# Optimization experiments

Measured on AMD Instinct MI355X. Metric: run time of the kernel, lower is better.

## Reference

```python
import jax, jax.numpy as jnp
import numpy as np

H = 64    # encoder/decoder hidden size
L = 10    # num_lags
D = 128   # input_dim (features)
OUT = 5   # out_dim
B = 8192


def lstm_cell(x, h, c, Wih, Whh, bih, bhh):
    # torch nn.LSTM gate order: i, f, g, o
    g = x @ Wih.T + bih + h @ Whh.T + bhh
    i, f, gg, o = jnp.split(g, 4, axis=-1)
    c = jax.nn.sigmoid(f) * c + jax.nn.sigmoid(i) * jnp.tanh(gg)
    h = jax.nn.sigmoid(o) * jnp.tanh(c)
    return h, c


def setup_inputs() -> dict:
    key = jax.random.key(0)
    ks = jax.random.split(key, 24)
    rn = lambda k, s, sc=0.05: jax.random.normal(k, s, jnp.float32) * sc
    return {
        "x": rn(ks[0], (B, L, D), 1.0),
        "y_hist": rn(ks[1], (B, L, OUT), 1.0),
        "h0_enc": rn(ks[2], (B, H), 0.1),
        "c0_enc": rn(ks[3], (B, H), 0.1),
        "h0_dec": rn(ks[4], (B, H), 0.1),
        "c0_dec": rn(ks[5], (B, H), 0.1),
        # encoder attention: Linear(2H+L -> 1)
        "enc_attn_w": rn(ks[6], (1, 2 * H + L)),
        "enc_attn_b": rn(ks[7], (1,)),
        # encoder LSTM
        "enc_Wih": rn(ks[8], (4 * H, D)),
        "enc_Whh": rn(ks[9], (4 * H, H)),
        "enc_bih": rn(ks[10], (4 * H,)),
        "enc_bhh": rn(ks[11], (4 * H,)),
        # decoder attention MLP: Linear(3H -> H), tanh, Linear(H -> 1)
        "dec_attn_w1": rn(ks[12], (H, 3 * H)),
        "dec_attn_b1": rn(ks[13], (H,)),
        "dec_attn_w2": rn(ks[14], (1, H)),
        "dec_attn_b2": rn(ks[15], (1,)),
        # decoder LSTM (input = out_dim)
        "dec_Wih": rn(ks[16], (4 * H, OUT)),
        "dec_Whh": rn(ks[17], (4 * H, H)),
        "dec_bih": rn(ks[18], (4 * H,)),
        "dec_bhh": rn(ks[19], (4 * H,)),
        # fc: Linear(H+OUT -> OUT)  (weight .normal_() in torch -> std 1)
        "fc_w": rn(ks[20], (OUT, H + OUT), 1.0),
        "fc_b": rn(ks[21], (OUT,)),
        # fc_out: Linear(2H -> OUT)
        "fcout_w": rn(ks[22], (OUT, 2 * H)),
        "fcout_b": rn(ks[23], (OUT,)),
    }


def reference(x, y_hist, h0_enc, c0_enc, h0_dec, c0_dec,
              enc_attn_w, enc_attn_b, enc_Wih, enc_Whh, enc_bih, enc_bhh,
              dec_attn_w1, dec_attn_b1, dec_attn_w2, dec_attn_b2,
              dec_Wih, dec_Whh, dec_bih, dec_bhh, fc_w, fc_b, fcout_w, fcout_b):
    # ---- encoder (input attention over features) ----
    # Linear([h; c; x_feat_series]) = wh.h + wc.c + wx.x_series + b
    wh, wc, wx = enc_attn_w[0, :H], enc_attn_w[0, H:2 * H], enc_attn_w[0, 2 * H:]
    score_x = jnp.einsum('bdl,l->bd', jnp.transpose(x, (0, 2, 1)), wx)  # [B, D]

    def enc_step(carry, x_t):
        h, c = carry
        scores = (h @ wh + c @ wc)[:, None] + score_x + enc_attn_b[0]   # [B, D]
        at = jax.nn.softmax(scores, axis=1)
        wi = at * x_t                                                   # [B, D]
        h, c = lstm_cell(wi, h, c, enc_Wih, enc_Whh, enc_bih, enc_bhh)
        return (h, c), h

    _, enc_seq = jax.lax.scan(enc_step, (h0_enc, c0_enc), jnp.transpose(x, (1, 0, 2)))
    x_enc = jnp.transpose(enc_seq, (1, 0, 2))                           # [B, L, H]

    # ---- decoder (temporal attention over encoded lags) ----
    W1h, W1c, W1x = dec_attn_w1[:, :H], dec_attn_w1[:, H:2 * H], dec_attn_w1[:, 2 * H:]
    pre = jnp.einsum('ble,he->blh', x_enc, W1x)                         # [B, L, H]
    w2 = dec_attn_w2[0]

    def dec_step(carry, y_t):
        h, c, _ = carry
        z = jnp.tanh(pre + (h @ W1h.T + c @ W1c.T + dec_attn_b1)[:, None, :])
        scores = z @ w2 + dec_attn_b2[0]                                # [B, L]
        at = jax.nn.softmax(scores, axis=1)
        ctx = jnp.einsum('bl,ble->be', at, x_enc)                       # [B, H]
        y_tilde = jnp.concatenate([ctx, y_t], axis=1) @ fc_w.T + fc_b   # [B, OUT]
        h, c = lstm_cell(y_tilde, h, c, dec_Wih, dec_Whh, dec_bih, dec_bhh)
        return (h, c, ctx), None

    (h, c, ctx), _ = jax.lax.scan(
        dec_step, (h0_dec, c0_dec, jnp.zeros_like(h0_dec)),
        jnp.transpose(y_hist, (1, 0, 2)))
    out = jnp.concatenate([h, ctx], axis=1) @ fcout_w.T + fcout_b       # [B, OUT]
    return out
```

## Files before the change

### kernel.cpp

```cpp
#include <hip/hip_runtime.h>

#define B_  8192
#define L_  10
#define D_  128
#define H_  64
#define OUT_ 5

typedef _Float16 h2 __attribute__((ext_vector_type(2)));
typedef _Float16 f16x8 __attribute__((ext_vector_type(8)));
typedef float f32x4 __attribute__((ext_vector_type(4)));
typedef unsigned int uint;

#define WS_ENCPK   0
#define WS_ENCB    24576
#define WS_DECY2   24832
#define WS_DECPK   26112
#define WS_DECB    34304
#define WS_W1HCP   34560
#define WS_W1XP    38656

__device__ __forceinline__ float sigmf(float x){ return 1.f/(1.f+__expf(-x)); }
__device__ __forceinline__ float tanhf_(float x){ return 1.f - 2.f/(1.f+__expf(2.f*x)); }
__device__ __forceinline__ uint pack_rtz(float a, float b){
  return __builtin_bit_cast(uint, __builtin_amdgcn_cvt_pkrtz(a, b));
}
__device__ __forceinline__ uint pack_rtn(float a, float b){
  h2 v; v.x = (_Float16)a; v.y = (_Float16)b;
  return __builtin_bit_cast(uint, v);
}
__device__ __forceinline__ float2 unpk(uint u){
  h2 v = __builtin_bit_cast(h2, u);
  return make_float2((float)v.x, (float)v.y);
}

union U4 { uint u[4]; uint4 q; f16x8 v; };

__global__ void prep_kernel(const float* __restrict__ encWih, const float* __restrict__ encWhh,
                            const float* __restrict__ encbih, const float* __restrict__ encbhh,
                            const float* __restrict__ decWih, const float* __restrict__ decWhh,
                            const float* __restrict__ decbih, const float* __restrict__ decbhh,
                            const float* __restrict__ w1, float* __restrict__ wsf)
{
  uint* ws = (uint*)wsf;
  int stride = gridDim.x * blockDim.x;
  int tid0 = blockIdx.x * blockDim.x + threadIdx.x;

  for (int idx = tid0; idx < 96*64; idx += stride) {
    int kp = idx >> 6, l = idx & 63;
    uint4 o; uint* op = (uint*)&o;
    #pragma unroll
    for (int q=0;q<4;++q){
      int j = q*64 + l;
      int k0 = 2*kp, k1 = 2*kp+1;
      float a = (k0 < 128) ? encWih[j*128 + k0] : encWhh[j*64 + (k0-128)];
      float b = (k1 < 128) ? encWih[j*128 + k1] : encWhh[j*64 + (k1-128)];
      op[q] = pack_rtn(a,b);
    }
    ((uint4*)(ws + WS_ENCPK))[idx] = o;
  }
  for (int idx = tid0; idx < 256; idx += stride) {
    int l = idx >> 2, q = idx & 3, j = q*64+l;
    wsf[WS_ENCB+idx] = encbih[j] + encbhh[j];
  }
  for (int idx = tid0; idx < 4*64; idx += stride) {
    int i = idx >> 6, l = idx & 63;
    uint4 o; uint* op = (uint*)&o;
    #pragma unroll
    for (int q=0;q<4;++q){
      int j = q*64 + l;
      int k0 = 2*i, k1 = 2*i+1;
      float a = (k0 < 5) ? decWih[j*5 + k0] : 0.f;
      float b = (k1 < 5) ? decWih[j*5 + k1] : 0.f;
      op[q] = pack_rtn(a,b);
    }
    ((uint4*)(ws + WS_DECY2))[idx] = o;
  }
  for (int idx = tid0; idx < 32*64; idx += stride) {
    int ep = idx >> 6, l = idx & 63;
    uint4 o; uint* op = (uint*)&o;
    #pragma unroll
    for (int q=0;q<4;++q){
      int j = q*64 + l;
      op[q] = pack_rtn(decWhh[j*64 + 2*ep], decWhh[j*64 + 2*ep+1]);
    }
    ((uint4*)(ws + WS_DECPK))[idx] = o;
  }
  for (int idx = tid0; idx < 256; idx += stride) {
    int l = idx >> 2, q = idx & 3, j = q*64+l;
    wsf[WS_DECB+idx] = decbih[j] + decbhh[j];
  }
  for (int idx = tid0; idx < 32*64; idx += stride) {
    int ep = idx >> 6, l = idx & 63;
    uint2 o;
    o.x = pack_rtn(w1[l*192 + 2*ep],      w1[l*192 + 2*ep+1]);
    o.y = pack_rtn(w1[l*192 + 64 + 2*ep], w1[l*192 + 64 + 2*ep+1]);
    ((uint2*)(ws + WS_W1HCP))[idx] = o;
  }
  for (int idx = tid0; idx < 32*64; idx += stride) {
    int ep = idx >> 6, l = idx & 63;
    ws[WS_W1XP + idx] = pack_rtn(w1[l*192 + 128 + 2*ep], w1[l*192 + 128 + 2*ep+1]);
  }
}

#define SM_HXE   0
#define SM_XES   4608
#define SM_TMPF  0
#define SM_TMPG  12800
#define SM_HXD   27648
#define SM_CXD   32256
#define SM_SRED  36864
#define SM_FXE   39424
#define SM_GXE   42624
#define SM_YBS   45824
#define SM_TOTAL 49024

__global__ __launch_bounds__(256, 2) void darnn_fused(
    const float* __restrict__ x, const float* __restrict__ enc_attn_w,
    const float* __restrict__ y_hist,
    const float* __restrict__ h0e, const float* __restrict__ c0e,
    const float* __restrict__ h0d, const float* __restrict__ c0d,
    const float* __restrict__ dec_attn_b1, const float* __restrict__ dec_attn_w2,
    const float* __restrict__ fc_w, const float* __restrict__ fc_b,
    const float* __restrict__ fcout_w, const float* __restrict__ fcout_b,
    const float* __restrict__ ws,
    float* __restrict__ out)
{
  const int tid = threadIdx.x;
  const int l   = tid & 63;
  const int w   = tid >> 6;
  const int col = l & 15;
  const int g   = l >> 4;
  const int b0  = blockIdx.x * 16;
  const int lw  = 16*w + col;
  const int u0  = 16*w + 4*g;

  const uint* wsu = (const uint*)ws;

  __shared__ __align__(16) char smem_[SM_TOTAL];
  _Float16 (*wiS)[16][136] = reinterpret_cast<_Float16(*)[16][136]>(smem_);
  uint     (*hxE)[16][36] = reinterpret_cast<uint(*)[16][36]>(smem_ + SM_HXE);
  _Float16 (*xeS)[16][72] = reinterpret_cast<_Float16(*)[16][72]>(smem_ + SM_XES);
  float* tmpF = (float*)(smem_ + SM_TMPF);
  float* tmpG = (float*)(smem_ + SM_TMPG);
  uint     (*hxD)[16][36] = reinterpret_cast<uint(*)[16][36]>(smem_ + SM_HXD);
  uint     (*cxD)[16][36] = reinterpret_cast<uint(*)[16][36]>(smem_ + SM_CXD);
  float* sred = (float*)(smem_ + SM_SRED);
  float* fxeS = (float*)(smem_ + SM_FXE);
  float* gxeS = (float*)(smem_ + SM_GXE);
  float* ybS  = (float*)(smem_ + SM_YBS);

  if (tid < 200){
    float4 yreg = *(const float4*)(y_hist + (size_t)b0*50 + tid*4);
    *(float4*)(ybS + tid*4) = yreg;
  }
  float4 hd4 = *(const float4*)(h0d + (size_t)(b0+col)*64 + u0);
  float4 cd4 = *(const float4*)(c0d + (size_t)(b0+col)*64 + u0);
  float4 he4 = *(const float4*)(h0e + (size_t)(b0+col)*64 + u0);
  float4 ce4 = *(const float4*)(c0e + (size_t)(b0+col)*64 + u0);

  f16x8 afr[4][4];
  #pragma unroll
  for (int im=0; im<4; ++im){
    #pragma unroll
    for (int kf=0; kf<4; ++kf){
      U4 cv;
      #pragma unroll
      for (int i=0;i<4;++i){
        int kp = kf*16 + g*4 + i;
        cv.u[i] = wsu[WS_ENCPK + (kp*64 + lw)*4 + im];
      }
      afr[im][kf] = cv.v;
    }
  }
  float bias[4][4];
  #pragma unroll
  for (int im=0; im<4; ++im)
    #pragma unroll
    for (int r=0; r<4; ++r)
      bias[im][r] = ws[WS_ENCB + (u0 + r)*4 + im];

  const int bb = tid >> 4;
  const int kc = tid & 15;
  const float* xb = x + (size_t)(b0+bb)*(L_*D_) + kc*8;

  float wxv[L_];
  #pragma unroll
  for (int t=0;t<L_;++t) wxv[t] = enc_attn_w[2*H_ + t];

  float s[8];
  #pragma unroll
  for (int j=0;j<8;++j) s[j]=0.f;
  #pragma unroll
  for (int t=0;t<L_;++t){
    float wx = wxv[t];
    float4 x0 = *(const float4*)(xb + t*D_);
    float4 x1 = *(const float4*)(xb + t*D_ + 4);
    s[0]+=x0.x*wx; s[1]+=x0.y*wx; s[2]+=x0.z*wx; s[3]+=x0.w*wx;
    s[4]+=x1.x*wx; s[5]+=x1.y*wx; s[6]+=x1.z*wx; s[7]+=x1.w*wx;
  }
  float m = s[0];
  #pragma unroll
  for (int j=1;j<8;++j) m = fmaxf(m, s[j]);
  m = fmaxf(m, __shfl_xor(m,1));
  m = fmaxf(m, __shfl_xor(m,2));
  m = fmaxf(m, __shfl_xor(m,4));
  m = fmaxf(m, __shfl_xor(m,8));
  float atw[8];
  float ss = 0.f;
  #pragma unroll
  for (int j=0;j<8;++j){ atw[j] = __expf(s[j]-m); ss += atw[j]; }
  ss += __shfl_xor(ss,1);
  ss += __shfl_xor(ss,2);
  ss += __shfl_xor(ss,4);
  ss += __shfl_xor(ss,8);
  float ainv = 1.f/ss;
  #pragma unroll
  for (int j=0;j<8;++j) atw[j] *= ainv;

  #pragma unroll
  for (int t=0;t<L_;++t){
    float4 x0 = *(const float4*)(xb + t*D_);
    float4 x1 = *(const float4*)(xb + t*D_ + 4);
    uint4 o;
    o.x = pack_rtz(atw[0]*x0.x, atw[1]*x0.y);
    o.y = pack_rtz(atw[2]*x0.z, atw[3]*x0.w);
    o.z = pack_rtz(atw[4]*x1.x, atw[5]*x1.y);
    o.w = pack_rtz(atw[6]*x1.z, atw[7]*x1.w);
    *(uint4*)&wiS[t][bb][kc*8] = o;
  }
  __syncthreads();

  uint2 gq[L_][4];
  #pragma unroll
  for (int t=0;t<L_;++t){
    U4 bu[4];
    #pragma unroll
    for (int kf=0;kf<4;++kf)
      bu[kf].q = *(const uint4*)&wiS[t][col][kf*32 + g*8];
    #pragma unroll
    for (int im=0;im<4;++im){
      f32x4 acc = { bias[im][0], bias[im][1], bias[im][2], bias[im][3] };
      #pragma unroll
      for (int kf=0;kf<4;++kf)
        acc = __builtin_amdgcn_mfma_f32_16x16x32_f16(afr[im][kf], bu[kf].v, acc, 0, 0, 0);
      gq[t][im] = make_uint2(pack_rtn(acc[0],acc[1]), pack_rtn(acc[2],acc[3]));
    }
  }
  __syncthreads();

  f16x8 aE[4][2];
  #pragma unroll
  for (int q=0;q<4;++q)
    #pragma unroll
    for (int kf=0;kf<2;++kf){
      U4 cv;
      #pragma unroll
      for (int i=0;i<4;++i)
        cv.u[i] = wsu[WS_ENCPK + ((64 + kf*16 + g*4 + i)*64 + lw)*4 + q];
      aE[q][kf] = cv.v;
    }

  float h[4], c[4], xer[L_][4];
  h[0]=he4.x; h[1]=he4.y; h[2]=he4.z; h[3]=he4.w;
  c[0]=ce4.x; c[1]=ce4.y; c[2]=ce4.z; c[3]=ce4.w;
  *(uint2*)&hxE[0][col][u0>>1] = make_uint2(pack_rtz(h[0],h[1]), pack_rtz(h[2],h[3]));
  __syncthreads();

  int p = 0;
  #pragma unroll
  for (int t=0; t<L_; ++t){
    f32x4 acc[4];
    #pragma unroll
    for (int q=0;q<4;++q){
      float2 u0f = unpk(gq[t][q].x), u1f = unpk(gq[t][q].y);
      acc[q][0]=u0f.x; acc[q][1]=u0f.y; acc[q][2]=u1f.x; acc[q][3]=u1f.y;
    }
    f16x8 hB[2];
    { U4 t0; t0.q = *(const uint4*)&hxE[p][col][g*4];      hB[0]=t0.v; }
    { U4 t1; t1.q = *(const uint4*)&hxE[p][col][16 + g*4]; hB[1]=t1.v; }

    #pragma unroll
    for (int q=0;q<4;++q){
      acc[q] = __builtin_amdgcn_mfma_f32_16x16x32_f16(aE[q][0], hB[0], acc[q], 0,0,0);
      acc[q] = __builtin_amdgcn_mfma_f32_16x16x32_f16(aE[q][1], hB[1], acc[q], 0,0,0);
    }
    #pragma unroll
    for (int r=0;r<4;++r){
      float ig=sigmf(acc[0][r]), fg=sigmf(acc[1][r]), gg=tanhf_(acc[2][r]), og=sigmf(acc[3][r]);
      c[r]=fg*c[r]+ig*gg;
      h[r]=og*tanhf_(c[r]);
      xer[t][r]=h[r];
    }
    uint2 hpk = make_uint2(pack_rtz(h[0],h[1]), pack_rtz(h[2],h[3]));
    *(uint2*)&xeS[t][col][u0] = hpk;
    *(uint2*)&hxE[p^1][col][u0>>1] = hpk;
    __syncthreads();
    p ^= 1;
  }

  f16x8 aX[2];
  #pragma unroll
  for (int kf=0;kf<2;++kf){
    U4 cv;
    #pragma unroll
    for (int i=0;i<4;++i) cv.u[i] = wsu[WS_W1XP + (kf*16 + g*4 + i)*64 + lw];
    aX[kf] = cv.v;
  }
  f32x4 preC[L_];
  #pragma unroll
  for (int lt=0;lt<L_;++lt){
    f32x4 a = {0.f,0.f,0.f,0.f};
    U4 bu0, bu1;
    bu0.q = *(const uint4*)&xeS[lt][col][g*8];
    bu1.q = *(const uint4*)&xeS[lt][col][32 + g*8];
    a = __builtin_amdgcn_mfma_f32_16x16x32_f16(aX[0], bu0.v, a, 0,0,0);
    a = __builtin_amdgcn_mfma_f32_16x16x32_f16(aX[1], bu1.v, a, 0,0,0);
    preC[lt] = a;
  }
  __syncthreads();

  {
    float fw1v[OUT_][4], gw1v[OUT_][4];
    #pragma unroll
    for (int o2=0;o2<OUT_;++o2)
      #pragma unroll
      for (int r=0;r<4;++r){
        fw1v[o2][r] = fc_w[o2*69 + u0 + r];
        gw1v[o2][r] = fcout_w[o2*128 + 64 + u0 + r];
      }
    #pragma unroll
    for (int lt=0;lt<L_;++lt){
      #pragma unroll
      for (int o2=0;o2<OUT_;++o2){
        float pf = fw1v[o2][0]*xer[lt][0] + fw1v[o2][1]*xer[lt][1]
                 + fw1v[o2][2]*xer[lt][2] + fw1v[o2][3]*xer[lt][3];
        float pg = gw1v[o2][0]*xer[lt][0] + gw1v[o2][1]*xer[lt][1]
                 + gw1v[o2][2]*xer[lt][2] + gw1v[o2][3]*xer[lt][3];
        pf += __shfl_xor(pf,16); pf += __shfl_xor(pf,32);
        pg += __shfl_xor(pg,16); pg += __shfl_xor(pg,32);
        if (g==0){
          tmpF[((lt*16+col)*OUT_+o2)*4 + w] = pf;
          tmpG[((lt*16+col)*OUT_+o2)*4 + w] = pg;
        }
      }
    }
  }
  __syncthreads();
  for (int idx=tid; idx<800; idx+=256){
    float4 f4 = *(const float4*)(tmpF + idx*4);
    float4 g4 = *(const float4*)(tmpG + idx*4);
    int o2 = idx % 5, rest = idx / 5;
    int b  = rest % 16, lt = rest / 16;
    fxeS[b*50 + lt*5 + o2] = f4.x+f4.y+f4.z+f4.w;
    gxeS[b*50 + lt*5 + o2] = g4.x+g4.y+g4.z+g4.w;
  }

  f16x8 aW1[4];
  #pragma unroll
  for (int kf=0;kf<4;++kf){
    U4 cv;
    #pragma unroll
    for (int i=0;i<4;++i){
      int ep = (kf&1)*16 + g*4 + i;
      cv.u[i] = wsu[WS_W1HCP + (ep*64 + lw)*2 + (kf>>1)];
    }
    aW1[kf] = cv.v;
  }
  f16x8 aGh[4][2];
  #pragma unroll
  for (int q=0;q<4;++q)
    #pragma unroll
    for (int kf=0;kf<2;++kf){
      U4 cv;
      #pragma unroll
      for (int i=0;i<4;++i)
        cv.u[i] = wsu[WS_DECPK + ((kf*16 + g*4 + i)*64 + lw)*4 + q];
      aGh[q][kf] = cv.v;
    }
  f16x8 aG0[4];
  #pragma unroll
  for (int q=0;q<4;++q){
    U4 cv;
    #pragma unroll
    for (int i=0;i<4;++i)
      cv.u[i] = (g==0) ? wsu[WS_DECY2 + (i*64 + lw)*4 + q] : 0u;
    aG0[q] = cv.v;
  }
  float4 bD[4];
  #pragma unroll
  for (int r=0;r<4;++r) bD[r] = *(const float4*)(ws + WS_DECB + (u0+r)*4);
  float4 b1v = *(const float4*)(dec_attn_b1 + u0);
  float4 w2v = *(const float4*)(dec_attn_w2 + u0);
  float fcbv[OUT_], fw2v[OUT_][OUT_];
  #pragma unroll
  for (int o2=0;o2<OUT_;++o2){
    fcbv[o2] = fc_b[o2];
    #pragma unroll
    for (int j=0;j<OUT_;++j) fw2v[o2][j] = fc_w[o2*69 + 64 + j];
  }

  h[0]=hd4.x; h[1]=hd4.y; h[2]=hd4.z; h[3]=hd4.w;
  c[0]=cd4.x; c[1]=cd4.y; c[2]=cd4.z; c[3]=cd4.w;
  *(uint2*)&hxD[0][col][u0>>1] = make_uint2(pack_rtz(h[0],h[1]), pack_rtz(h[2],h[3]));
  *(uint2*)&cxD[0][col][u0>>1] = make_uint2(pack_rtz(c[0],c[1]), pack_rtz(c[2],c[3]));
  __syncthreads();

  float at[L_];
  float inv = 0.f;
  p = 0;
  for (int t=0; t<L_; ++t){
    f16x8 hB[2], cB[2];
    { U4 t0; t0.q = *(const uint4*)&hxD[p][col][g*4];      hB[0]=t0.v; }
    { U4 t1; t1.q = *(const uint4*)&hxD[p][col][16 + g*4]; hB[1]=t1.v; }
    { U4 t2; t2.q = *(const uint4*)&cxD[p][col][g*4];      cB[0]=t2.v; }
    { U4 t3; t3.q = *(const uint4*)&cxD[p][col][16 + g*4]; cB[1]=t3.v; }

    f32x4 vb = { b1v.x, b1v.y, b1v.z, b1v.w };
    vb = __builtin_amdgcn_mfma_f32_16x16x32_f16(aW1[0], hB[0], vb, 0,0,0);
    vb = __builtin_amdgcn_mfma_f32_16x16x32_f16(aW1[1], hB[1], vb, 0,0,0);
    vb = __builtin_amdgcn_mfma_f32_16x16x32_f16(aW1[2], cB[0], vb, 0,0,0);
    vb = __builtin_amdgcn_mfma_f32_16x16x32_f16(aW1[3], cB[1], vb, 0,0,0);

    #pragma unroll
    for (int lt=0;lt<L_;++lt){
      float zp = tanhf_(preC[lt][0] + vb[0]) * w2v.x
               + tanhf_(preC[lt][1] + vb[1]) * w2v.y
               + tanhf_(preC[lt][2] + vb[2]) * w2v.z
               + tanhf_(preC[lt][3] + vb[3]) * w2v.w;
      zp += __shfl_xor(zp,16);
      zp += __shfl_xor(zp,32);
      at[lt] = zp;
    }
    if (g==0){
      #pragma unroll
      for (int lt=0;lt<L_;++lt) sred[(lt*16+col)*4 + w] = at[lt];
    }
    __syncthreads();
    #pragma unroll
    for (int lt=0;lt<L_;++lt){
      float4 s4 = *(const float4*)(sred + (lt*16+col)*4);
      at[lt] = s4.x + s4.y + s4.z + s4.w;
    }
    float mx = at[0];
    #pragma unroll
    for (int lt=1;lt<L_;++lt) mx = fmaxf(mx, at[lt]);
    float ssum = 0.f;
    #pragma unroll
    for (int lt=0;lt<L_;++lt){ at[lt] = __expf(at[lt]-mx); ssum += at[lt]; }
    inv = 1.f/ssum;

    U4 ycv; ycv.u[0]=0u; ycv.u[1]=0u; ycv.u[2]=0u; ycv.u[3]=0u;
    if (g==0){
      const float* fx = fxeS + col*50;
      const float* yb = ybS + col*50 + t*5;
      float yt[OUT_];
      #pragma unroll
      for (int o2=0;o2<OUT_;++o2){
        float sv = 0.f;
        #pragma unroll
        for (int lt=0;lt<L_;++lt) sv += at[lt]*fx[lt*5+o2];
        float v = sv*inv + fcbv[o2];
        #pragma unroll
        for (int j=0;j<OUT_;++j) v += yb[j]*fw2v[o2][j];
        yt[o2] = v;
      }
      ycv.u[0] = pack_rtn(yt[0], yt[1]);
      ycv.u[1] = pack_rtn(yt[2], yt[3]);
      ycv.u[2] = pack_rtn(yt[4], 0.f);
    }
    f32x4 accQ[4];
    #pragma unroll
    for (int q=0;q<4;++q){
      accQ[q][0]=((const float*)&bD[0])[q];
      accQ[q][1]=((const float*)&bD[1])[q];
      accQ[q][2]=((const float*)&bD[2])[q];
      accQ[q][3]=((const float*)&bD[3])[q];
    }
    #pragma unroll
    for (int q=0;q<4;++q){
      accQ[q] = __builtin_amdgcn_mfma_f32_16x16x32_f16(aG0[q], ycv.v, accQ[q], 0,0,0);
      accQ[q] = __builtin_amdgcn_mfma_f32_16x16x32_f16(aGh[q][0], hB[0], accQ[q], 0,0,0);
      accQ[q] = __builtin_amdgcn_mfma_f32_16x16x32_f16(aGh[q][1], hB[1], accQ[q], 0,0,0);
    }
    #pragma unroll
    for (int r=0;r<4;++r){
      float ig=sigmf(accQ[0][r]), fg=sigmf(accQ[1][r]), gg=tanhf_(accQ[2][r]), og=sigmf(accQ[3][r]);
      c[r]=fg*c[r]+ig*gg;
      h[r]=og*tanhf_(c[r]);
    }
    *(uint2*)&hxD[p^1][col][u0>>1] = make_uint2(pack_rtz(h[0],h[1]), pack_rtz(h[2],h[3]));
    *(uint2*)&cxD[p^1][col][u0>>1] = make_uint2(pack_rtz(c[0],c[1]), pack_rtz(c[2],c[3]));
    __syncthreads();
    p ^= 1;
  }

  {
    float fcA[OUT_][4];
    #pragma unroll
    for (int o2=0;o2<OUT_;++o2)
      #pragma unroll
      for (int r=0;r<4;++r) fcA[o2][r] = fcout_w[o2*128 + u0 + r];
    #pragma unroll
    for (int o2=0;o2<OUT_;++o2){
      float pv = fcA[o2][0]*h[0] + fcA[o2][1]*h[1] + fcA[o2][2]*h[2] + fcA[o2][3]*h[3];
      pv += __shfl_xor(pv,16);
      pv += __shfl_xor(pv,32);
      if (g==0) sred[(o2*16+col)*4 + w] = pv;
    }
  }
  __syncthreads();
  if (w==0 && g==0){
    const float* gx = gxeS + col*50;
    #pragma unroll
    for (int o2=0;o2<OUT_;++o2){
      float4 s4 = *(const float4*)(sred + (o2*16+col)*4);
      float sv = 0.f;
      #pragma unroll
      for (int lt=0;lt<L_;++lt) sv += at[lt]*gx[lt*5+o2];
      out[(size_t)(b0+col)*OUT_ + o2] = s4.x+s4.y+s4.z+s4.w + sv*inv + fcout_b[o2];
    }
  }
}

extern "C" void kernel_launch(void* const* d_in, const int* in_sizes, int n_in,
                              void* d_out, int out_size, void* d_ws, size_t ws_size,
                              hipStream_t stream) {
  const float* x          = (const float*)d_in[0];
  const float* y_hist     = (const float*)d_in[1];
  const float* h0_enc     = (const float*)d_in[2];
  const float* c0_enc     = (const float*)d_in[3];
  const float* h0_dec     = (const float*)d_in[4];
  const float* c0_dec     = (const float*)d_in[5];
  const float* enc_attn_w = (const float*)d_in[6];
  const float* enc_Wih    = (const float*)d_in[8];
  const float* enc_Whh    = (const float*)d_in[9];
  const float* enc_bih    = (const float*)d_in[10];
  const float* enc_bhh    = (const float*)d_in[11];
  const float* dec_attn_w1= (const float*)d_in[12];
  const float* dec_attn_b1= (const float*)d_in[13];
  const float* dec_attn_w2= (const float*)d_in[14];
  const float* dec_Wih    = (const float*)d_in[16];
  const float* dec_Whh    = (const float*)d_in[17];
  const float* dec_bih    = (const float*)d_in[18];
  const float* dec_bhh    = (const float*)d_in[19];
  const float* fc_w       = (const float*)d_in[20];
  const float* fc_b       = (const float*)d_in[21];
  const float* fcout_w    = (const float*)d_in[22];
  const float* fcout_b    = (const float*)d_in[23];
  float* ws = (float*)d_ws;
  float* out = (float*)d_out;

  hipLaunchKernelGGL(prep_kernel, dim3(128), dim3(256), 0, stream,
                     enc_Wih, enc_Whh, enc_bih, enc_bhh,
                     dec_Wih, dec_Whh, dec_bih, dec_bhh,
                     dec_attn_w1, ws);
  hipLaunchKernelGGL(darnn_fused, dim3(B_/16), dim3(256), 0, stream,
                     x, enc_attn_w, y_hist,
                     h0_enc, c0_enc, h0_dec, c0_dec,
                     dec_attn_b1, dec_attn_w2,
                     fc_w, fc_b, fcout_w, fcout_b, ws, out);
}
```

Before: 220.6 us.

## Fuse encoder input projection into recurrent loop and stage x in two halves

The separate pass that computed all ten timesteps' input-gate projections into registers (stored as packed fp16) is removed. Each recurrent step now runs the input MFMAs and the hidden MFMAs together in fp32 accumulation. Weighted x is staged in shared memory five timesteps at a time, so the LDS buffer is halved, and the second half is loaded after the first five steps. This drops the big gq register array and an fp16 rounding of the gate preactivations, at the cost of a longer serial critical path per step, since the input MFMAs now sit inside the recurrence, plus a slightly larger LDS footprint.

```diff
diff --git a/kernel.cpp b/kernel.cpp
--- a/kernel.cpp
+++ b/kernel.cpp
@@ -28,10 +28,6 @@
   h2 v; v.x = (_Float16)a; v.y = (_Float16)b;
   return __builtin_bit_cast(uint, v);
 }
-__device__ __forceinline__ float2 unpk(uint u){
-  h2 v = __builtin_bit_cast(h2, u);
-  return make_float2((float)v.x, (float)v.y);
-}
 
 union U4 { uint u[4]; uint4 q; f16x8 v; };
 
@@ -102,17 +98,18 @@
   }
 }
 
-#define SM_HXE   0
-#define SM_XES   4608
+#define SM_WIS   0
+#define SM_HXE   21760
+#define SM_XES   26368
+#define SM_YBS   49408
 #define SM_TMPF  0
 #define SM_TMPG  12800
-#define SM_HXD   27648
-#define SM_CXD   32256
-#define SM_SRED  36864
-#define SM_FXE   39424
-#define SM_GXE   42624
-#define SM_YBS   45824
-#define SM_TOTAL 49024
+#define SM_HXD   25600
+#define SM_CXD   30208
+#define SM_SRED  34816
+#define SM_FXE   37376
+#define SM_GXE   40576
+#define SM_TOTAL 52608
 
 __global__ __launch_bounds__(256, 2) void darnn_fused(
     const float* __restrict__ x, const float* __restrict__ enc_attn_w,
@@ -137,7 +134,7 @@
   const uint* wsu = (const uint*)ws;
 
   __shared__ __align__(16) char smem_[SM_TOTAL];
-  _Float16 (*wiS)[16][136] = reinterpret_cast<_Float16(*)[16][136]>(smem_);
+  _Float16 (*wiS)[16][136] = reinterpret_cast<_Float16(*)[16][136]>(smem_ + SM_WIS);
   uint     (*hxE)[16][36] = reinterpret_cast<uint(*)[16][36]>(smem_ + SM_HXE);
   _Float16 (*xeS)[16][72] = reinterpret_cast<_Float16(*)[16][72]>(smem_ + SM_XES);
   float* tmpF = (float*)(smem_ + SM_TMPF);
@@ -172,6 +169,17 @@
       afr[im][kf] = cv.v;
     }
   }
+  f16x8 aE[4][2];
+  #pragma unroll
+  for (int q=0;q<4;++q)
+    #pragma unroll
+    for (int kf=0;kf<2;++kf){
+      U4 cv;
+      #pragma unroll
+      for (int i=0;i<4;++i)
+        cv.u[i] = wsu[WS_ENCPK + ((64 + kf*16 + g*4 + i)*64 + lw)*4 + q];
+      aE[q][kf] = cv.v;
+    }
   float bias[4][4];
   #pragma unroll
   for (int im=0; im<4; ++im)
@@ -218,7 +226,7 @@
   for (int j=0;j<8;++j) atw[j] *= ainv;
 
   #pragma unroll
-  for (int t=0;t<L_;++t){
+  for (int t=0;t<5;++t){
     float4 x0 = *(const float4*)(xb + t*D_);
     float4 x1 = *(const float4*)(xb + t*D_ + 4);
     uint4 o;
@@ -228,37 +236,6 @@
     o.w = pack_rtz(atw[6]*x1.z, atw[7]*x1.w);
     *(uint4*)&wiS[t][bb][kc*8] = o;
   }
-  __syncthreads();
-
-  uint2 gq[L_][4];
-  #pragma unroll
-  for (int t=0;t<L_;++t){
-    U4 bu[4];
-    #pragma unroll
-    for (int kf=0;kf<4;++kf)
-      bu[kf].q = *(const uint4*)&wiS[t][col][kf*32 + g*8];
-    #pragma unroll
-    for (int im=0;im<4;++im){
-      f32x4 acc = { bias[im][0], bias[im][1], bias[im][2], bias[im][3] };
-      #pragma unroll
-      for (int kf=0;kf<4;++kf)
-        acc = __builtin_amdgcn_mfma_f32_16x16x32_f16(afr[im][kf], bu[kf].v, acc, 0, 0, 0);
-      gq[t][im] = make_uint2(pack_rtn(acc[0],acc[1]), pack_rtn(acc[2],acc[3]));
-    }
-  }
-  __syncthreads();
-
-  f16x8 aE[4][2];
-  #pragma unroll
-  for (int q=0;q<4;++q)
-    #pragma unroll
-    for (int kf=0;kf<2;++kf){
-      U4 cv;
-      #pragma unroll
-      for (int i=0;i<4;++i)
-        cv.u[i] = wsu[WS_ENCPK + ((64 + kf*16 + g*4 + i)*64 + lw)*4 + q];
-      aE[q][kf] = cv.v;
-    }
 
   float h[4], c[4], xer[L_][4];
   h[0]=he4.x; h[1]=he4.y; h[2]=he4.z; h[3]=he4.w;
@@ -268,34 +245,59 @@
 
   int p = 0;
   #pragma unroll
-  for (int t=0; t<L_; ++t){
-    f32x4 acc[4];
-    #pragma unroll
-    for (int q=0;q<4;++q){
-      float2 u0f = unpk(gq[t][q].x), u1f = unpk(gq[t][q].y);
-      acc[q][0]=u0f.x; acc[q][1]=u0f.y; acc[q][2]=u1f.x; acc[q][3]=u1f.y;
-    }
-    f16x8 hB[2];
-    { U4 t0; t0.q = *(const uint4*)&hxE[p][col][g*4];      hB[0]=t0.v; }
-    { U4 t1; t1.q = *(const uint4*)&hxE[p][col][16 + g*4]; hB[1]=t1.v; }
-
-    #pragma unroll
-    for (int q=0;q<4;++q){
-      acc[q] = __builtin_amdgcn_mfma_f32_16x16x32_f16(aE[q][0], hB[0], acc[q], 0,0,0);
-      acc[q] = __builtin_amdgcn_mfma_f32_16x16x32_f16(aE[q][1], hB[1], acc[q], 0,0,0);
-    }
-    #pragma unroll
-    for (int r=0;r<4;++r){
-      float ig=sigmf(acc[0][r]), fg=sigmf(acc[1][r]), gg=tanhf_(acc[2][r]), og=sigmf(acc[3][r]);
-      c[r]=fg*c[r]+ig*gg;
-      h[r]=og*tanhf_(c[r]);
-      xer[t][r]=h[r];
-    }
-    uint2 hpk = make_uint2(pack_rtz(h[0],h[1]), pack_rtz(h[2],h[3]));
-    *(uint2*)&xeS[t][col][u0] = hpk;
-    *(uint2*)&hxE[p^1][col][u0>>1] = hpk;
-    __syncthreads();
-    p ^= 1;
+  for (int half=0; half<2; ++half){
+    #pragma unroll
+    for (int tt=0; tt<5; ++tt){
+      const int t = half*5 + tt;
+      U4 bu[4];
+      #pragma unroll
+      for (int kf=0;kf<4;++kf)
+        bu[kf].q = *(const uint4*)&wiS[tt][col][kf*32 + g*8];
+      f16x8 hB[2];
+      { U4 t0; t0.q = *(const uint4*)&hxE[p][col][g*4];      hB[0]=t0.v; }
+      { U4 t1; t1.q = *(const uint4*)&hxE[p][col][16 + g*4]; hB[1]=t1.v; }
+
+      f32x4 acc[4];
+      #pragma unroll
+      for (int q=0;q<4;++q){
+        acc[q][0]=bias[q][0]; acc[q][1]=bias[q][1];
+        acc[q][2]=bias[q][2]; acc[q][3]=bias[q][3];
+      }
+      #pragma unroll
+      for (int q=0;q<4;++q){
+        #pragma unroll
+        for (int kf=0;kf<4;++kf)
+          acc[q] = __builtin_amdgcn_mfma_f32_16x16x32_f16(afr[q][kf], bu[kf].v, acc[q], 0,0,0);
+        acc[q] = __builtin_amdgcn_mfma_f32_16x16x32_f16(aE[q][0], hB[0], acc[q], 0,0,0);
+        acc[q] = __builtin_amdgcn_mfma_f32_16x16x32_f16(aE[q][1], hB[1], acc[q], 0,0,0);
+      }
+      #pragma unroll
+      for (int r=0;r<4;++r){
+        float ig=sigmf(acc[0][r]), fg=sigmf(acc[1][r]), gg=tanhf_(acc[2][r]), og=sigmf(acc[3][r]);
+        c[r]=fg*c[r]+ig*gg;
+        h[r]=og*tanhf_(c[r]);
+        xer[t][r]=h[r];
+      }
+      uint2 hpk = make_uint2(pack_rtz(h[0],h[1]), pack_rtz(h[2],h[3]));
+      *(uint2*)&xeS[t][col][u0] = hpk;
+      *(uint2*)&hxE[p^1][col][u0>>1] = hpk;
+      __syncthreads();
+      p ^= 1;
+    }
+    if (half==0){
+      #pragma unroll
+      for (int t=5;t<L_;++t){
+        float4 x0 = *(const float4*)(xb + t*D_);
+        float4 x1 = *(const float4*)(xb + t*D_ + 4);
+        uint4 o;
+        o.x = pack_rtz(atw[0]*x0.x, atw[1]*x0.y);
+        o.y = pack_rtz(atw[2]*x0.z, atw[3]*x0.w);
+        o.z = pack_rtz(atw[4]*x1.x, atw[5]*x1.y);
+        o.w = pack_rtz(atw[6]*x1.z, atw[7]*x1.w);
+        *(uint4*)&wiS[t-5][bb][kc*8] = o;
+      }
+      __syncthreads();
+    }
   }
 
   f16x8 aX[2];
@@ -317,7 +319,6 @@
     a = __builtin_amdgcn_mfma_f32_16x16x32_f16(aX[1], bu1.v, a, 0,0,0);
     preC[lt] = a;
   }
-  __syncthreads();
 
   {
     float fw1v[OUT_][4], gw1v[OUT_][4];
```

Result: faster. 214.8 us (-2.6%).
